# Optimization experiments

Measured on AMD Instinct MI355X. Metric: run time of the kernel, lower is better.

## Reference

```python
import jax, jax.numpy as jnp
import numpy as np

D_MODEL = 1024
D_KEY = 64
BATCH = 4
SEQ = 4096


def setup_inputs() -> dict:
    key = jax.random.key(0)
    kq, kk, kv, kwq, kwk, kwv = jax.random.split(key, 6)
    queries = jax.random.normal(kq, (BATCH, SEQ, D_MODEL), dtype=jnp.float32)
    keys = jax.random.normal(kk, (BATCH, SEQ, D_MODEL), dtype=jnp.float32)
    values = jax.random.normal(kv, (BATCH, SEQ, D_MODEL), dtype=jnp.float32)
    # causal mask: 1 = keep, 0 = masked out (torch masked_fill where mask==0)
    mask = jnp.tril(jnp.ones((SEQ, SEQ), dtype=jnp.int32))
    s = 1.0 / np.sqrt(D_MODEL)
    Wq = jax.random.normal(kwq, (D_MODEL, D_KEY), dtype=jnp.float32) * s
    Wk = jax.random.normal(kwk, (D_MODEL, D_KEY), dtype=jnp.float32) * s
    Wv = jax.random.normal(kwv, (D_MODEL, D_KEY), dtype=jnp.float32) * s
    return {"queries": queries, "keys": keys, "values": values,
            "mask": mask, "Wq": Wq, "Wk": Wk, "Wv": Wv}


def reference(queries, keys, values, mask, Wq, Wk, Wv):
    q = jnp.einsum('bsd,dk->bsk', queries, Wq)   # [B,S,dk]
    k = jnp.einsum('bsd,dk->bsk', keys, Wk)
    v = jnp.einsum('bsd,dk->bsk', values, Wv)
    scale = 1.0 / np.sqrt(D_KEY).astype(np.float32)
    attn = jnp.einsum('bqk,bsk->bqs', q, k) * scale  # [B,Sq,Sk]
    attn = jnp.where(mask == 0, -jnp.inf, attn)
    attn = jax.nn.softmax(attn, axis=-1)
    return jnp.einsum('bqs,bsk->bqk', attn, v)      # [B,S,dk]
```

## Files before the change

### kernel.cpp

```cpp
#include <hip/hip_runtime.h>
#include <hip/hip_bf16.h>

#define B      4
#define SEQ    4096
#define DM     1024
#define DK     64
#define NSPLIT 8

typedef __bf16 bf16x8 __attribute__((ext_vector_type(8)));
typedef __bf16 bf16x4 __attribute__((ext_vector_type(4)));
typedef float  f32x4  __attribute__((ext_vector_type(4)));

#define KSTR 72
#define ASTR 1032

#define QSCALE 0.1803368801111204f
#define M2BIAS 12.0f

__global__ __launch_bounds__(256) void wt_kernel(
    const float* __restrict__ Wq, const float* __restrict__ Wk,
    const float* __restrict__ Wv, __bf16* __restrict__ Wt)
{
    const int mat = blockIdx.y;
    const float* W = (mat == 0) ? Wq : (mat == 1) ? Wk : Wv;
    const float scale = (mat == 0) ? QSCALE : 1.0f;
    const int k0 = blockIdx.x * 64;
    const int tid = threadIdx.x;

    __shared__ float t[64][65];

    const int r = tid >> 2;
    const int c = (tid & 3) * 16;
    {
        const float* src = W + (size_t)(k0 + r) * DK + c;
        #pragma unroll
        for (int j = 0; j < 4; ++j) {
            float4 a = *(const float4*)(src + j * 4);
            t[r][c + j * 4 + 0] = a.x; t[r][c + j * 4 + 1] = a.y;
            t[r][c + j * 4 + 2] = a.z; t[r][c + j * 4 + 3] = a.w;
        }
    }
    __syncthreads();
    const int n  = tid >> 2;
    const int kk = (tid & 3) * 16;
    bf16x8 b0, b1;
    #pragma unroll
    for (int j = 0; j < 8; ++j) b0[j] = (__bf16)(t[kk + j][n] * scale);
    #pragma unroll
    for (int j = 0; j < 8; ++j) b1[j] = (__bf16)(t[kk + 8 + j][n] * scale);
    __bf16* dst = Wt + (size_t)(mat * DK + n) * DM + k0 + kk;
    *(bf16x8*)(dst)     = b0;
    *(bf16x8*)(dst + 8) = b1;
}

__global__ __launch_bounds__(256) void proj_strip_kernel(
    const float* __restrict__ q_in, const float* __restrict__ k_in,
    const float* __restrict__ v_in, const __bf16* __restrict__ Wt,
    __bf16* __restrict__ qb, __bf16* __restrict__ kb,
    __bf16* __restrict__ vtb)
{
    const int m = blockIdx.y;
    const float* in = (m == 0) ? q_in : (m == 1) ? k_in : v_in;
    const __bf16* wt = Wt + (size_t)m * DK * DM;

    const int rowbase = blockIdx.x * 16;
    const int tid  = threadIdx.x;
    const int w    = tid >> 6;
    const int lane = tid & 63;
    const int quad = lane >> 4;
    const int l15  = lane & 15;

    __shared__ char SM[16 * ASTR * 2];
    __bf16* As = (__bf16*)SM;
    float*  Rs = (float*)SM;

    const float* src = in + (size_t)rowbase * DM;
    float4 ld[16];
    #pragma unroll
    for (int i = 0; i < 16; ++i)
        ld[i] = *(const float4*)(src + i * 1024 + tid * 4);
    #pragma unroll
    for (int i = 0; i < 16; ++i) {
        bf16x4 b;
        b[0] = (__bf16)ld[i].x; b[1] = (__bf16)ld[i].y;
        b[2] = (__bf16)ld[i].z; b[3] = (__bf16)ld[i].w;
        *(bf16x4*)&As[i * ASTR + tid * 4] = b;
    }
    __syncthreads();

    f32x4 acc[4];
    #pragma unroll
    for (int nf = 0; nf < 4; ++nf) acc[nf] = (f32x4){0.f, 0.f, 0.f, 0.f};

    const int kbase = w * 256;
    #pragma unroll
    for (int j = 0; j < 8; ++j) {
        const int kc = kbase + j * 32;
        bf16x8 af = *(const bf16x8*)&As[l15 * ASTR + kc + quad * 8];
        #pragma unroll
        for (int nf = 0; nf < 4; ++nf) {
            bf16x8 wb = *(const bf16x8*)(wt + (size_t)(nf * 16 + l15) * DM + kc + quad * 8);
            acc[nf] = __builtin_amdgcn_mfma_f32_16x16x32_bf16(af, wb, acc[nf], 0, 0, 0);
        }
    }
    __syncthreads();

    #pragma unroll
    for (int nf = 0; nf < 4; ++nf)
        #pragma unroll
        for (int r = 0; r < 4; ++r)
            Rs[(w * 16 + quad * 4 + r) * 64 + nf * 16 + l15] = acc[nf][r];
    __syncthreads();

    if (m < 2) {
        __bf16* outb = (m == 0) ? qb : kb;
        const int c  = tid & 63;
        const int r0 = tid >> 6;
        #pragma unroll
        for (int rr = 0; rr < 4; ++rr) {
            const int r = r0 + rr * 4;
            const float o = Rs[r * 64 + c] + Rs[1024 + r * 64 + c] +
                            Rs[2048 + r * 64 + c] + Rs[3072 + r * 64 + c];
            outb[(size_t)(rowbase + r) * DK + c] = (__bf16)o;
        }
    } else {
        const int c2 = tid >> 2;
        const int x  = tid & 3;
        const int bb = rowbase >> 12;
        const int s0 = rowbase & (SEQ - 1);
        bf16x4 v4;
        #pragma unroll
        for (int y = 0; y < 4; ++y) {
            const int s = x * 4 + y;
            const float o = Rs[s * 64 + c2] + Rs[1024 + s * 64 + c2] +
                            Rs[2048 + s * 64 + c2] + Rs[3072 + s * 64 + c2];
            v4[y] = (__bf16)o;
        }
        *(bf16x4*)&vtb[(size_t)(bb * DK + c2) * SEQ + s0 + x * 4] = v4;
    }
}

__global__ __launch_bounds__(256) void flash_kernel(
    const __bf16* __restrict__ qb, const __bf16* __restrict__ kb,
    const __bf16* __restrict__ vtb, __bf16* __restrict__ Opart,
    float* __restrict__ lpart)
{
    const int qt  = blockIdx.x;
    const int bb  = blockIdx.y;
    const int z   = blockIdx.z;
    const int tid = threadIdx.x;
    const int w    = tid >> 6;
    const int lane = tid & 63;
    const int quad = lane >> 4;
    const int l15  = lane & 15;

    __shared__ __bf16 Ps[4][2][16 * KSTR];

    const int qrow_base = qt * 128 + w * 32;
    const int niters = 2 * qt + 2;
    const int kt0 = (niters * z) / NSPLIT;
    const int kt1 = (niters * (z + 1)) / NSPLIT;

    bf16x8 qf[2][2];
    #pragma unroll
    for (int g = 0; g < 2; ++g) {
        const __bf16* qp = qb + ((size_t)(bb * SEQ + qrow_base + g * 16 + l15)) * DK + quad * 8;
        qf[g][0] = *(const bf16x8*)(qp);
        qf[g][1] = *(const bf16x8*)(qp + 32);
    }

    bf16x8 ones;
    #pragma unroll
    for (int j = 0; j < 8; ++j) ones[j] = (__bf16)1.0f;

    f32x4 of[2][4], lacc[2];
    #pragma unroll
    for (int g = 0; g < 2; ++g) {
        #pragma unroll
        for (int nf = 0; nf < 4; ++nf) of[g][nf] = (f32x4){0.f, 0.f, 0.f, 0.f};
        lacc[g] = (f32x4){0.f, 0.f, 0.f, 0.f};
    }

    const __bf16* kB = kb  + (size_t)bb * SEQ * DK + (size_t)l15 * DK + quad * 8;
    const __bf16* vB = vtb + (size_t)bb * DK * SEQ + (size_t)l15 * SEQ + quad * 8;

    for (int kt = kt0; kt < kt1; ++kt) {
        bf16x8 kf[4][2];
        #pragma unroll
        for (int nf = 0; nf < 4; ++nf) {
            const __bf16* kp = kB + (size_t)(kt * 64 + nf * 16) * DK;
            kf[nf][0] = *(const bf16x8*)(kp);
            kf[nf][1] = *(const bf16x8*)(kp + 32);
        }

        f32x4 sf[2][4];
        #pragma unroll
        for (int g = 0; g < 2; ++g)
            #pragma unroll
            for (int nf = 0; nf < 4; ++nf)
                sf[g][nf] = (f32x4){-M2BIAS, -M2BIAS, -M2BIAS, -M2BIAS};
        #pragma unroll
        for (int nf = 0; nf < 4; ++nf) {
            #pragma unroll
            for (int ch = 0; ch < 2; ++ch) {
                sf[0][nf] = __builtin_amdgcn_mfma_f32_16x16x32_bf16(qf[0][ch], kf[nf][ch], sf[0][nf], 0, 0, 0);
                sf[1][nf] = __builtin_amdgcn_mfma_f32_16x16x32_bf16(qf[1][ch], kf[nf][ch], sf[1][nf], 0, 0, 0);
            }
        }

        bf16x8 vf[4][2];
        #pragma unroll
        for (int nf = 0; nf < 4; ++nf) {
            const __bf16* vp = vB + (size_t)(nf * 16) * SEQ + kt * 64;
            vf[nf][0] = *(const bf16x8*)(vp);
            vf[nf][1] = *(const bf16x8*)(vp + 32);
        }

        const int kc0 = kt * 64;
        #pragma unroll
        for (int g = 0; g < 2; ++g) {
            const int r0 = qrow_base + g * 16;
            const bool dg = (kc0 + 63 > r0);
            #pragma unroll
            for (int nf = 0; nf < 4; ++nf) {
                #pragma unroll
                for (int r = 0; r < 4; ++r) {
                    float s = sf[g][nf][r];
                    if (dg) {
                        const int col = kc0 + nf * 16 + l15;
                        const int row = r0 + quad * 4 + r;
                        if (col > row) s = -1.0e9f;
                    }
                    const float p = __builtin_amdgcn_exp2f(s);
                    Ps[w][g][(quad * 4 + r) * KSTR + nf * 16 + l15] = (__bf16)p;
                }
            }
        }

        bf16x8 pf[2][2];
        #pragma unroll
        for (int g = 0; g < 2; ++g) {
            pf[g][0] = *(const bf16x8*)(&Ps[w][g][l15 * KSTR + quad * 8]);
            pf[g][1] = *(const bf16x8*)(&Ps[w][g][l15 * KSTR + 32 + quad * 8]);
            lacc[g] = __builtin_amdgcn_mfma_f32_16x16x32_bf16(pf[g][0], ones, lacc[g], 0, 0, 0);
            lacc[g] = __builtin_amdgcn_mfma_f32_16x16x32_bf16(pf[g][1], ones, lacc[g], 0, 0, 0);
        }

        #pragma unroll
        for (int nf = 0; nf < 4; ++nf) {
            #pragma unroll
            for (int ch = 0; ch < 2; ++ch) {
                of[0][nf] = __builtin_amdgcn_mfma_f32_16x16x32_bf16(pf[0][ch], vf[nf][ch], of[0][nf], 0, 0, 0);
                of[1][nf] = __builtin_amdgcn_mfma_f32_16x16x32_bf16(pf[1][ch], vf[nf][ch], of[1][nf], 0, 0, 0);
            }
        }
    }

    #pragma unroll
    for (int g = 0; g < 2; ++g) {
        __bf16* Op = Opart + ((size_t)(z * B + bb) * SEQ + qrow_base + g * 16) * DK;
        #pragma unroll
        for (int nf = 0; nf < 4; ++nf)
            #pragma unroll
            for (int r = 0; r < 4; ++r)
                Op[(size_t)(quad * 4 + r) * DK + nf * 16 + l15] = (__bf16)of[g][nf][r];
        if (l15 == 0) {
            const size_t base = (size_t)(z * B + bb) * SEQ + qrow_base + g * 16 + quad * 4;
            #pragma unroll
            for (int r = 0; r < 4; ++r)
                lpart[base + r] = lacc[g][r];
        }
    }
}

__global__ __launch_bounds__(256) void combine_kernel(
    const __bf16* __restrict__ Opart, const float* __restrict__ lpart,
    float* __restrict__ out)
{
    const int idx = blockIdx.x * 256 + threadIdx.x;
    const int row = idx >> 6;

    float L = 0.f, o = 0.f;
    #pragma unroll
    for (int z = 0; z < NSPLIT; ++z) {
        L += lpart[(size_t)z * (B * SEQ) + row];
        o += (float)Opart[(size_t)z * (B * SEQ) * DK + idx];
    }
    out[idx] = o / L;
}

extern "C" void kernel_launch(void* const* d_in, const int* in_sizes, int n_in,
                              void* d_out, int out_size, void* d_ws, size_t ws_size,
                              hipStream_t stream)
{
    const float* queries = (const float*)d_in[0];
    const float* keys    = (const float*)d_in[1];
    const float* values  = (const float*)d_in[2];
    const float* Wq = (const float*)d_in[4];
    const float* Wk = (const float*)d_in[5];
    const float* Wv = (const float*)d_in[6];
    float* out = (float*)d_out;

    char* p = (char*)d_ws;
    __bf16* qb  = (__bf16*)p;  p += (size_t)B * SEQ * DK * 2;
    __bf16* kb  = (__bf16*)p;  p += (size_t)B * SEQ * DK * 2;
    __bf16* vtb = (__bf16*)p;  p += (size_t)B * SEQ * DK * 2;
    __bf16* Wt  = (__bf16*)p;  p += (size_t)3 * DK * DM * 2;
    __bf16* Opart = (__bf16*)p; p += (size_t)NSPLIT * B * SEQ * DK * 2;
    float* lpart = (float*)p;   p += (size_t)NSPLIT * B * SEQ * 4;

    wt_kernel<<<dim3(DM / 64, 3), 256, 0, stream>>>(Wq, Wk, Wv, Wt);

    proj_strip_kernel<<<dim3((B * SEQ) / 16, 3), 256, 0, stream>>>(
        queries, keys, values, Wt, qb, kb, vtb);

    flash_kernel<<<dim3(SEQ / 128, B, NSPLIT), 256, 0, stream>>>(
        qb, kb, vtb, Opart, lpart);

    combine_kernel<<<(B * SEQ * DK) / 256, 256, 0, stream>>>(
        Opart, lpart, out);
}
```

Baseline: 317.8 us.

## Load projection inputs straight to LDS and pre-swizzle V for coalesced flash loads

The projection kernel now moves fp32 input rows directly from global memory into LDS with global_load_lds and a rotated (swizzled) chunk order, and converts to bf16 only when building MFMA fragments. This drops the register round-trip and the separate bf16 LDS store. The V projection output is written in a fragment-ordered layout so that each flash-kernel lane reads contiguous 16-byte chunks per tile instead of strided rows of a transposed V. In exchange, LDS use per block grows to 64KB, which may lower occupancy.

```diff
diff --git a/kernel.cpp b/kernel.cpp
--- a/kernel.cpp
+++ b/kernel.cpp
@@ -1,5 +1,6 @@
 #include <hip/hip_runtime.h>
 #include <hip/hip_bf16.h>
+#include <stdint.h>
 
 #define B      4
 #define SEQ    4096
@@ -12,10 +13,15 @@
 typedef float  f32x4  __attribute__((ext_vector_type(4)));
 
 #define KSTR 72
-#define ASTR 1032
 
 #define QSCALE 0.1803368801111204f
 #define M2BIAS 12.0f
+
+__device__ __forceinline__ void load_lds16(const void* g, void* l) {
+    __builtin_amdgcn_global_load_lds(
+        (const __attribute__((address_space(1))) unsigned int*)g,
+        (__attribute__((address_space(3))) unsigned int*)l, 16, 0, 0);
+}
 
 __global__ __launch_bounds__(256) void wt_kernel(
     const float* __restrict__ Wq, const float* __restrict__ Wk,
@@ -53,11 +59,11 @@
     *(bf16x8*)(dst + 8) = b1;
 }
 
-__global__ __launch_bounds__(256) void proj_strip_kernel(
+__global__ __launch_bounds__(256) void proj_kernel(
     const float* __restrict__ q_in, const float* __restrict__ k_in,
     const float* __restrict__ v_in, const __bf16* __restrict__ Wt,
     __bf16* __restrict__ qb, __bf16* __restrict__ kb,
-    __bf16* __restrict__ vtb)
+    __bf16* __restrict__ V2)
 {
     const int m = blockIdx.y;
     const float* in = (m == 0) ? q_in : (m == 1) ? k_in : v_in;
@@ -70,21 +76,15 @@
     const int quad = lane >> 4;
     const int l15  = lane & 15;
 
-    __shared__ char SM[16 * ASTR * 2];
-    __bf16* As = (__bf16*)SM;
-    float*  Rs = (float*)SM;
-
-    const float* src = in + (size_t)rowbase * DM;
-    float4 ld[16];
-    #pragma unroll
-    for (int i = 0; i < 16; ++i)
-        ld[i] = *(const float4*)(src + i * 1024 + tid * 4);
-    #pragma unroll
-    for (int i = 0; i < 16; ++i) {
-        bf16x4 b;
-        b[0] = (__bf16)ld[i].x; b[1] = (__bf16)ld[i].y;
-        b[2] = (__bf16)ld[i].z; b[3] = (__bf16)ld[i].w;
-        *(bf16x4*)&As[i * ASTR + tid * 4] = b;
+    __shared__ char SM[65536];
+    char* wreg = SM + (w << 14);
+
+    const char* strip = (const char*)in + (size_t)rowbase * (DM * 4) + w * 1024;
+    #pragma unroll
+    for (int r = 0; r < 16; ++r) {
+        const int src_chunk = (lane - r) & 63;
+        load_lds16(strip + (size_t)r * 4096 + src_chunk * 16,
+                   wreg + r * 1024);
     }
     __syncthreads();
 
@@ -92,24 +92,33 @@
     #pragma unroll
     for (int nf = 0; nf < 4; ++nf) acc[nf] = (f32x4){0.f, 0.f, 0.f, 0.f};
 
-    const int kbase = w * 256;
+    const char* Arow = wreg + l15 * 1024;
+    const int cb = quad * 2 + l15;
     #pragma unroll
     for (int j = 0; j < 8; ++j) {
-        const int kc = kbase + j * 32;
-        bf16x8 af = *(const bf16x8*)&As[l15 * ASTR + kc + quad * 8];
+        const int pa = ((j * 8 + cb) & 63) * 16;
+        const int pb = ((j * 8 + 1 + cb) & 63) * 16;
+        float4 f0 = *(const float4*)(Arow + pa);
+        float4 f1 = *(const float4*)(Arow + pb);
+        bf16x8 af;
+        af[0] = (__bf16)f0.x; af[1] = (__bf16)f0.y;
+        af[2] = (__bf16)f0.z; af[3] = (__bf16)f0.w;
+        af[4] = (__bf16)f1.x; af[5] = (__bf16)f1.y;
+        af[6] = (__bf16)f1.z; af[7] = (__bf16)f1.w;
+        const int kc = w * 256 + j * 32;
         #pragma unroll
         for (int nf = 0; nf < 4; ++nf) {
             bf16x8 wb = *(const bf16x8*)(wt + (size_t)(nf * 16 + l15) * DM + kc + quad * 8);
             acc[nf] = __builtin_amdgcn_mfma_f32_16x16x32_bf16(af, wb, acc[nf], 0, 0, 0);
         }
     }
-    __syncthreads();
-
+
+    float* RsW = (float*)(SM + (w << 14));
     #pragma unroll
     for (int nf = 0; nf < 4; ++nf)
         #pragma unroll
         for (int r = 0; r < 4; ++r)
-            Rs[(w * 16 + quad * 4 + r) * 64 + nf * 16 + l15] = acc[nf][r];
+            RsW[(quad * 4 + r) * 64 + nf * 16 + l15] = acc[nf][r];
     __syncthreads();
 
     if (m < 2) {
@@ -119,30 +128,41 @@
         #pragma unroll
         for (int rr = 0; rr < 4; ++rr) {
             const int r = r0 + rr * 4;
-            const float o = Rs[r * 64 + c] + Rs[1024 + r * 64 + c] +
-                            Rs[2048 + r * 64 + c] + Rs[3072 + r * 64 + c];
+            float o = 0.f;
+            #pragma unroll
+            for (int w2 = 0; w2 < 4; ++w2)
+                o += ((const float*)(SM + (w2 << 14)))[r * 64 + c];
             outb[(size_t)(rowbase + r) * DK + c] = (__bf16)o;
         }
     } else {
-        const int c2 = tid >> 2;
+        const int n  = tid >> 2;
         const int x  = tid & 3;
         const int bb = rowbase >> 12;
         const int s0 = rowbase & (SEQ - 1);
+        const int p0 = s0 + x * 4;
+        const int kt = p0 >> 6;
+        const int ch = (p0 >> 5) & 1;
+        const int qg = (p0 >> 3) & 3;
+        const int j0 = p0 & 7;
         bf16x4 v4;
         #pragma unroll
         for (int y = 0; y < 4; ++y) {
-            const int s = x * 4 + y;
-            const float o = Rs[s * 64 + c2] + Rs[1024 + s * 64 + c2] +
-                            Rs[2048 + s * 64 + c2] + Rs[3072 + s * 64 + c2];
+            const int i = x * 4 + y;
+            float o = 0.f;
+            #pragma unroll
+            for (int w2 = 0; w2 < 4; ++w2)
+                o += ((const float*)(SM + (w2 << 14)))[i * 64 + n];
             v4[y] = (__bf16)o;
         }
-        *(bf16x4*)&vtb[(size_t)(bb * DK + c2) * SEQ + s0 + x * 4] = v4;
+        const size_t e = (size_t)bb * 262144 + (size_t)kt * 4096 + ch * 2048 +
+                         (n >> 4) * 512 + qg * 128 + (n & 15) * 8 + j0;
+        *(bf16x4*)&V2[e] = v4;
     }
 }
 
 __global__ __launch_bounds__(256) void flash_kernel(
     const __bf16* __restrict__ qb, const __bf16* __restrict__ kb,
-    const __bf16* __restrict__ vtb, __bf16* __restrict__ Opart,
+    const __bf16* __restrict__ V2, __bf16* __restrict__ Opart,
     float* __restrict__ lpart)
 {
     const int qt  = blockIdx.x;
@@ -181,8 +201,8 @@
         lacc[g] = (f32x4){0.f, 0.f, 0.f, 0.f};
     }
 
-    const __bf16* kB = kb  + (size_t)bb * SEQ * DK + (size_t)l15 * DK + quad * 8;
-    const __bf16* vB = vtb + (size_t)bb * DK * SEQ + (size_t)l15 * SEQ + quad * 8;
+    const __bf16* kB  = kb + (size_t)bb * SEQ * DK + (size_t)l15 * DK + quad * 8;
+    const __bf16* v2B = V2 + (size_t)bb * 262144 + (size_t)lane * 8;
 
     for (int kt = kt0; kt < kt1; ++kt) {
         bf16x8 kf[4][2];
@@ -211,9 +231,9 @@
         bf16x8 vf[4][2];
         #pragma unroll
         for (int nf = 0; nf < 4; ++nf) {
-            const __bf16* vp = vB + (size_t)(nf * 16) * SEQ + kt * 64;
-            vf[nf][0] = *(const bf16x8*)(vp);
-            vf[nf][1] = *(const bf16x8*)(vp + 32);
+            #pragma unroll
+            for (int ch = 0; ch < 2; ++ch)
+                vf[nf][ch] = *(const bf16x8*)(v2B + (size_t)kt * 4096 + ch * 2048 + nf * 512);
         }
 
         const int kc0 = kt * 64;
@@ -304,18 +324,18 @@
     char* p = (char*)d_ws;
     __bf16* qb  = (__bf16*)p;  p += (size_t)B * SEQ * DK * 2;
     __bf16* kb  = (__bf16*)p;  p += (size_t)B * SEQ * DK * 2;
-    __bf16* vtb = (__bf16*)p;  p += (size_t)B * SEQ * DK * 2;
+    __bf16* V2  = (__bf16*)p;  p += (size_t)B * SEQ * DK * 2;
     __bf16* Wt  = (__bf16*)p;  p += (size_t)3 * DK * DM * 2;
     __bf16* Opart = (__bf16*)p; p += (size_t)NSPLIT * B * SEQ * DK * 2;
     float* lpart = (float*)p;   p += (size_t)NSPLIT * B * SEQ * 4;
 
     wt_kernel<<<dim3(DM / 64, 3), 256, 0, stream>>>(Wq, Wk, Wv, Wt);
 
-    proj_strip_kernel<<<dim3((B * SEQ) / 16, 3), 256, 0, stream>>>(
-        queries, keys, values, Wt, qb, kb, vtb);
+    proj_kernel<<<dim3((B * SEQ) / 16, 3), 256, 0, stream>>>(
+        queries, keys, values, Wt, qb, kb, V2);
 
     flash_kernel<<<dim3(SEQ / 128, B, NSPLIT), 256, 0, stream>>>(
-        qb, kb, vtb, Opart, lpart);
+        qb, kb, V2, Opart, lpart);
 
     combine_kernel<<<(B * SEQ * DK) / 256, 256, 0, stream>>>(
         Opart, lpart, out);
```

New measurement: 321.2 us. About the same (+1.1%).
